# Performance work log

Measured on AMD Instinct MI355X. Metric: run time of the kernel, lower is better.

The kernel has to match this reference:

```python
import jax, jax.numpy as jnp
import numpy as np

N_NODES = 50000
N_EDGES = 800000
NODE_DIM = 64
EDGE_DIM = 32
OUT_FEATS = 64


def setup_inputs() -> dict:
    key = jax.random.key(0)
    k1, k2, k3, k4, k5, k6, k7 = jax.random.split(key, 7)
    node_features = jax.random.normal(k1, (N_NODES, NODE_DIM), dtype=jnp.float32)
    edge_features = jax.random.normal(k2, (N_EDGES, EDGE_DIM), dtype=jnp.float32)
    src = jax.random.randint(k3, (N_EDGES,), 0, N_NODES, dtype=jnp.int32)
    dst = jax.random.randint(k4, (N_EDGES,), 0, N_NODES, dtype=jnp.int32)
    in_dim = 2 * NODE_DIM + EDGE_DIM  # concat([e_ft, h_src, h_dst])
    w_group = jax.random.normal(k5, (in_dim,), dtype=jnp.float32) * 0.05
    w_srcattn = jax.random.normal(k6, (NODE_DIM + EDGE_DIM,), dtype=jnp.float32) * 0.05
    w_lin = jax.random.normal(k7, (in_dim, OUT_FEATS), dtype=jnp.float32) * 0.05
    return {"node_features": node_features, "edge_features": edge_features,
            "src": src, "dst": dst,
            "w_group": w_group, "w_srcattn": w_srcattn, "w_lin": w_lin}


def _segment_softmax(scores, seg, num_segments):
    # numerically-stable softmax of per-edge scalar scores within each segment
    m = jax.ops.segment_max(scores, seg, num_segments=num_segments)
    e = jnp.exp(scores - m[seg])
    s = jax.ops.segment_sum(e, seg, num_segments=num_segments)
    return e / s[seg]


def reference(node_features, edge_features, src, dst, w_group, w_srcattn, w_lin):
    h = node_features              # [N, node_dim]
    e_ft = edge_features           # [E, edge_dim]
    h_src = h[src]                 # [E, node_dim]
    h_dst = h[dst]                 # [E, node_dim]

    # --- group_apply_edges(group_by='src'): edge attention over out-edges of each src ---
    z2 = jnp.concatenate([e_ft, h_src, h_dst], axis=1)      # [E, edge_dim + 2*node_dim]
    a = z2 @ w_group                                        # [E]
    gamma = _segment_softmax(a, src, N_NODES)               # softmax over edges sharing src
    e_weighted = gamma[:, None] * e_ft                      # [E, edge_dim]

    # --- gnn_msg: msg = concat([h_src, e_weighted]) ---
    msg = jnp.concatenate([h_src, e_weighted], axis=1)      # [E, node_dim + edge_dim]

    # --- gnn_reduce: attention softmax over mailbox (edges sharing dst), weighted sum ---
    s = msg @ w_srcattn                                     # [E]
    alpha = _segment_softmax(s, dst, N_NODES)
    accum = jax.ops.segment_sum(alpha[:, None] * msg, dst, num_segments=N_NODES)  # [N, node_dim+edge_dim]

    # --- node_update: linear(concat([h, accum])) + relu ---
    h_cat = jnp.concatenate([h, accum], axis=1)             # [N, 2*node_dim + edge_dim]
    out = jax.nn.relu(h_cat @ w_lin)                        # [N, out_feats]
    return out
```

## Files before the change

kernel.cpp:

```cpp
#include <hip/hip_runtime.h>

#define NN 50000
#define NE 800000
#define NHB 3125
#define NTILES 3125

typedef __attribute__((ext_vector_type(8))) short bf16x8;
typedef __attribute__((ext_vector_type(4))) float f32x4;

static __device__ __forceinline__ short f2bf(float f) {
    unsigned int u = __float_as_uint(f);
    u += 0x7FFFu + ((u >> 16) & 1u);
    return (short)(u >> 16);
}

__global__ __launch_bounds__(256) void k_pre(
    const float* __restrict__ h, const int* __restrict__ dst,
    const float* __restrict__ wg, const float* __restrict__ wa,
    int* __restrict__ cnt, int* __restrict__ rank,
    float* __restrict__ p1, float* __restrict__ pd, float* __restrict__ dpf)
{
    int tid = threadIdx.x;
    if (blockIdx.x < NHB) {
        int e = blockIdx.x * 256 + tid;
        if (e < NE) rank[e] = atomicAdd(&cnt[dst[e]], 1);
        return;
    }
    __shared__ float4 ls[16], ld[16], lt[16];
    if (tid < 16)      ls[tid]      = ((const float4*)wg)[8 + tid];
    else if (tid < 32) ld[tid - 16] = ((const float4*)wg)[8 + tid];
    else if (tid < 48) lt[tid - 32] = ((const float4*)wa)[tid - 32];
    __syncthreads();
    int n = (blockIdx.x - NHB) * 16 + (tid >> 4);
    if (n >= NN) return;
    int l16 = tid & 15;
    float4 v = ((const float4*)(h + (size_t)n * 64))[l16];
    float4 w1 = ls[l16], w2 = ld[l16], w3 = lt[l16];
    float s1 = v.x*w1.x + v.y*w1.y + v.z*w1.z + v.w*w1.w;
    float s2 = v.x*w2.x + v.y*w2.y + v.z*w2.z + v.w*w2.w;
    float s3 = v.x*w3.x + v.y*w3.y + v.z*w3.z + v.w*w3.w;
    #pragma unroll
    for (int m = 8; m; m >>= 1) {
        s1 += __shfl_xor(s1, m);
        s2 += __shfl_xor(s2, m);
        s3 += __shfl_xor(s3, m);
    }
    if (l16 == 0) { p1[n] = s1; pd[n] = s2; dpf[2 * n + 1] = s3; }
}

__global__ __launch_bounds__(256) void k_assign(
    const int* __restrict__ cnt, int* __restrict__ off, int* __restrict__ gtotal)
{
    int n = blockIdx.x * 256 + threadIdx.x;
    int lane = threadIdx.x & 63;
    int c = (n < NN) ? cnt[n] : 0;
    int pre = c;
    #pragma unroll
    for (int d = 1; d < 64; d <<= 1) {
        int v = __shfl_up(pre, d);
        if (lane >= d) pre += v;
    }
    int base = 0;
    if (lane == 63) base = atomicAdd(gtotal, pre);
    base = __shfl(base, 63);
    if (n < NN) off[n] = base + pre - c;
}

__global__ __launch_bounds__(256) void k_edge(
    const float* __restrict__ ef, const int* __restrict__ src,
    const int* __restrict__ dst, const int* __restrict__ rank,
    const float* __restrict__ wg, const float* __restrict__ wa,
    const float* __restrict__ p1, const float* __restrict__ pd,
    float* __restrict__ dpf, const int* __restrict__ off,
    int4* __restrict__ recA)
{
    __shared__ float4 lwe[8], lae[8];
    int tid = threadIdx.x;
    if (tid < 8)       lwe[tid]     = ((const float4*)wg)[tid];
    else if (tid < 16) lae[tid - 8] = ((const float4*)wa)[tid - 8 + 16];
    __syncthreads();
    int e = blockIdx.x * 256 + tid;
    if (e >= NE) return;
    int s = src[e], d = dst[e], rk = rank[e];
    const float4* e4 = (const float4*)(ef + (size_t)e * 32);
    float a = 0.f, u = 0.f;
    #pragma unroll
    for (int q = 0; q < 8; ++q) {
        float4 v = e4[q], w = lwe[q], w2 = lae[q];
        a += v.x*w.x  + v.y*w.y  + v.z*w.z  + v.w*w.w;
        u += v.x*w2.x + v.y*w2.y + v.z*w2.z + v.w*w2.w;
    }
    a += p1[s] + pd[d];
    float eav = __expf(a);
    atomicAdd(&dpf[2 * s], eav);
    int pos = off[d] + rk;
    recA[pos] = make_int4(s, e, __float_as_int(eav), __float_as_int(u));
}

__global__ __launch_bounds__(256) void k_reduce(
    const float* __restrict__ h, const float* __restrict__ ef,
    const int* __restrict__ cnt, const int* __restrict__ off,
    const float2* __restrict__ dp, const int4* __restrict__ recA,
    float* __restrict__ accum)
{
    int n = blockIdx.x * 4 + (threadIdx.x >> 6);
    if (n >= NN) return;
    int lane = threadIdx.x & 63;
    bool up = lane >= 32;
    int l5 = lane & 31;
    int deg = cnt[n], base = off[n];
    float acch = 0.f, acce = 0.f, den = 0.f;
    int j = 0;
    for (; j + 4 <= deg; j += 4) {
        int4 r0 = recA[base+j+0], r1 = recA[base+j+1];
        int4 r2 = recA[base+j+2], r3 = recA[base+j+3];
        float2 d0 = dp[r0.x], d1 = dp[r1.x], d2 = dp[r2.x], d3 = dp[r3.x];
        float h0 = h[(size_t)r0.x*64+lane], h1 = h[(size_t)r1.x*64+lane];
        float h2 = h[(size_t)r2.x*64+lane], h3 = h[(size_t)r3.x*64+lane];
        int eA = up ? r1.y : r0.y, eB = up ? r3.y : r2.y;
        float efA = ef[(size_t)eA*32 + l5];
        float efB = ef[(size_t)eB*32 + l5];
        float g0 = __int_as_float(r0.z)/d0.x, g1 = __int_as_float(r1.z)/d1.x;
        float g2 = __int_as_float(r2.z)/d2.x, g3 = __int_as_float(r3.z)/d3.x;
        float s0 = __expf(d0.y + g0*__int_as_float(r0.w));
        float s1 = __expf(d1.y + g1*__int_as_float(r1.w));
        float s2 = __expf(d2.y + g2*__int_as_float(r2.w));
        float s3 = __expf(d3.y + g3*__int_as_float(r3.w));
        den  += s0 + s1 + s2 + s3;
        acch += s0*h0 + s1*h1 + s2*h2 + s3*h3;
        float wA = up ? s1*g1 : s0*g0;
        float wB = up ? s3*g3 : s2*g2;
        acce += wA*efA + wB*efB;
    }
    for (; j < deg; ++j) {
        int4 r = recA[base+j];
        float2 dt = dp[r.x];
        float g = __int_as_float(r.z)/dt.x;
        float s = __expf(dt.y + g*__int_as_float(r.w));
        den += s;
        acch += s * h[(size_t)r.x*64+lane];
        if (!up) acce += s * g * ef[(size_t)r.y*32 + l5];
    }
    acce += __shfl_xor(acce, 32);
    float inv = (deg > 0) ? 1.f/den : 0.f;
    accum[(size_t)n*96 + lane] = acch * inv;
    if (!up) accum[(size_t)n*96 + 64 + lane] = acce * inv;
}

__global__ __launch_bounds__(256) void k_node_update(
    const float* __restrict__ h, const float* __restrict__ accum,
    const float* __restrict__ wl_g, float* __restrict__ out)
{
    int lane = threadIdx.x & 63;
    int col  = lane & 15;
    int quad = lane >> 4;
    int wid  = blockIdx.x * 4 + (threadIdx.x >> 6);
    int nwaves = gridDim.x * 4;

    bf16x8 bfr[5][4];
    #pragma unroll
    for (int kc = 0; kc < 5; ++kc)
        #pragma unroll
        for (int nt = 0; nt < 4; ++nt) {
            #pragma unroll
            for (int j = 0; j < 8; ++j) {
                int k = kc * 32 + quad * 8 + j;
                bfr[kc][nt][j] = f2bf(wl_g[k * 64 + nt * 16 + col]);
            }
        }

    for (int tile = wid; tile < NTILES; tile += nwaves) {
        int n = tile * 16 + col;
        f32x4 acc[4];
        #pragma unroll
        for (int nt = 0; nt < 4; ++nt) acc[nt] = (f32x4){0.f, 0.f, 0.f, 0.f};

        #pragma unroll
        for (int kc = 0; kc < 5; ++kc) {
            int kbase = kc * 32 + quad * 8;
            const float* p = (kbase < 64)
                ? (h     + (size_t)n * 64 + kbase)
                : (accum + (size_t)n * 96 + (kbase - 64));
            float4 va = *(const float4*)p;
            float4 vb = *(const float4*)(p + 4);
            bf16x8 af;
            af[0] = f2bf(va.x); af[1] = f2bf(va.y);
            af[2] = f2bf(va.z); af[3] = f2bf(va.w);
            af[4] = f2bf(vb.x); af[5] = f2bf(vb.y);
            af[6] = f2bf(vb.z); af[7] = f2bf(vb.w);
            #pragma unroll
            for (int nt = 0; nt < 4; ++nt)
                acc[nt] = __builtin_amdgcn_mfma_f32_16x16x32_bf16(
                    af, bfr[kc][nt], acc[nt], 0, 0, 0);
        }

        #pragma unroll
        for (int nt = 0; nt < 4; ++nt) {
            #pragma unroll
            for (int r = 0; r < 4; ++r) {
                int node = tile * 16 + quad * 4 + r;
                out[(size_t)node * 64 + nt * 16 + col] = fmaxf(acc[nt][r], 0.f);
            }
        }
    }
}

extern "C" void kernel_launch(void* const* d_in, const int* in_sizes, int n_in,
                              void* d_out, int out_size, void* d_ws, size_t ws_size,
                              hipStream_t stream)
{
    const float* h   = (const float*)d_in[0];
    const float* ef  = (const float*)d_in[1];
    const int*   src = (const int*)d_in[2];
    const int*   dst = (const int*)d_in[3];
    const float* wg  = (const float*)d_in[4];
    const float* wa  = (const float*)d_in[5];
    const float* wl  = (const float*)d_in[6];
    float* out = (float*)d_out;

    float* ws = (float*)d_ws;
    float*  dpf    = ws;
    int*    cnt    = (int*)(ws + 2 * NN);
    int*    gtotal = (int*)(ws + 3 * NN);
    int*    off    = (int*)(ws + 3 * NN + 16);
    float*  p1     = ws + 4 * NN + 16;
    float*  pd     = ws + 5 * NN + 16;
    int4*   recA   = (int4*)(ws + 6 * NN + 16);
    int*    rank   = (int*)(ws + 6 * NN + 16 + 4 * NE);
    float*  accum  = ws + 6 * NN + 16 + 4 * NE;

    hipMemsetAsync(d_ws, 0, (size_t)(3 * NN + 16) * sizeof(float), stream);

    k_pre<<<2 * NHB, 256, 0, stream>>>(h, dst, wg, wa, cnt, rank, p1, pd, dpf);
    k_assign<<<(NN + 255) / 256, 256, 0, stream>>>(cnt, off, gtotal);
    k_edge<<<NHB, 256, 0, stream>>>(ef, src, dst, rank, wg, wa, p1, pd, dpf,
                                    off, recA);
    k_reduce<<<(NN + 3) / 4, 256, 0, stream>>>(h, ef, cnt, off, (const float2*)dpf,
                                               recA, accum);
    k_node_update<<<256, 256, 0, stream>>>(h, accum, wl, out);
}
```

Baseline: 336.6 us.

## Precompute per-edge softmax weights in a rewrite pass and move edge dots into pre-kernel

The edge-feature dot products (attention score part and srcattn part) move into the first kernel as a third block range, so they run alongside the degree histogram and are stored as a float2 per edge. A new k_rewrite pass runs once per record after the src-softmax denominators are complete. It computes gamma and exp(s) and stores exp(s) and exp(s)*gamma in recA. This removes the per-record dp gather, divide and exp from the reduce loop, where all 64 lanes of a wave repeated them. In exchange it adds an extra kernel launch, extra global traffic for the au buffer, and a full read-modify-write of recA. Bounds checks are also dropped because the sizes divide evenly.

Measured after the change: 346.2 us. 2.9% more time.

```diff
diff --git a/kernel.cpp b/kernel.cpp
--- a/kernel.cpp
+++ b/kernel.cpp
@@ -3,7 +3,6 @@
 #define NN 50000
 #define NE 800000
 #define NHB 3125
-#define NTILES 3125
 
 typedef __attribute__((ext_vector_type(8))) short bf16x8;
 typedef __attribute__((ext_vector_type(4))) float f32x4;
@@ -15,37 +14,55 @@
 }
 
 __global__ __launch_bounds__(256) void k_pre(
-    const float* __restrict__ h, const int* __restrict__ dst,
+    const float* __restrict__ h, const float* __restrict__ ef,
+    const int* __restrict__ dst,
     const float* __restrict__ wg, const float* __restrict__ wa,
     int* __restrict__ cnt, int* __restrict__ rank,
-    float* __restrict__ p1, float* __restrict__ pd, float* __restrict__ dpf)
+    float* __restrict__ p1, float* __restrict__ pd, float* __restrict__ dpf,
+    float2* __restrict__ au)
 {
     int tid = threadIdx.x;
     if (blockIdx.x < NHB) {
         int e = blockIdx.x * 256 + tid;
-        if (e < NE) rank[e] = atomicAdd(&cnt[dst[e]], 1);
+        rank[e] = atomicAdd(&cnt[dst[e]], 1);
         return;
     }
-    __shared__ float4 ls[16], ld[16], lt[16];
-    if (tid < 16)      ls[tid]      = ((const float4*)wg)[8 + tid];
-    else if (tid < 32) ld[tid - 16] = ((const float4*)wg)[8 + tid];
-    else if (tid < 48) lt[tid - 32] = ((const float4*)wa)[tid - 32];
+    if (blockIdx.x < 2 * NHB) {
+        __shared__ float4 ls[16], ld[16], lt[16];
+        if (tid < 16)      ls[tid]      = ((const float4*)wg)[8 + tid];
+        else if (tid < 32) ld[tid - 16] = ((const float4*)wg)[8 + tid];
+        else if (tid < 48) lt[tid - 32] = ((const float4*)wa)[tid - 32];
+        __syncthreads();
+        int n = (blockIdx.x - NHB) * 16 + (tid >> 4);
+        int l16 = tid & 15;
+        float4 v = ((const float4*)(h + (size_t)n * 64))[l16];
+        float4 w1 = ls[l16], w2 = ld[l16], w3 = lt[l16];
+        float s1 = v.x*w1.x + v.y*w1.y + v.z*w1.z + v.w*w1.w;
+        float s2 = v.x*w2.x + v.y*w2.y + v.z*w2.z + v.w*w2.w;
+        float s3 = v.x*w3.x + v.y*w3.y + v.z*w3.z + v.w*w3.w;
+        #pragma unroll
+        for (int m = 8; m; m >>= 1) {
+            s1 += __shfl_xor(s1, m);
+            s2 += __shfl_xor(s2, m);
+            s3 += __shfl_xor(s3, m);
+        }
+        if (l16 == 0) { p1[n] = s1; pd[n] = s2; dpf[2 * n + 1] = s3; }
+        return;
+    }
+    __shared__ float4 lwe[8], lae[8];
+    if (tid < 8)       lwe[tid]     = ((const float4*)wg)[tid];
+    else if (tid < 16) lae[tid - 8] = ((const float4*)wa)[tid - 8 + 16];
     __syncthreads();
-    int n = (blockIdx.x - NHB) * 16 + (tid >> 4);
-    if (n >= NN) return;
-    int l16 = tid & 15;
-    float4 v = ((const float4*)(h + (size_t)n * 64))[l16];
-    float4 w1 = ls[l16], w2 = ld[l16], w3 = lt[l16];
-    float s1 = v.x*w1.x + v.y*w1.y + v.z*w1.z + v.w*w1.w;
-    float s2 = v.x*w2.x + v.y*w2.y + v.z*w2.z + v.w*w2.w;
-    float s3 = v.x*w3.x + v.y*w3.y + v.z*w3.z + v.w*w3.w;
+    int e = (blockIdx.x - 2 * NHB) * 256 + tid;
+    const float4* e4 = (const float4*)(ef + (size_t)e * 32);
+    float a = 0.f, u = 0.f;
     #pragma unroll
-    for (int m = 8; m; m >>= 1) {
-        s1 += __shfl_xor(s1, m);
-        s2 += __shfl_xor(s2, m);
-        s3 += __shfl_xor(s3, m);
-    }
-    if (l16 == 0) { p1[n] = s1; pd[n] = s2; dpf[2 * n + 1] = s3; }
+    for (int q = 0; q < 8; ++q) {
+        float4 v = e4[q], w = lwe[q], w2 = lae[q];
+        a += v.x*w.x  + v.y*w.y  + v.z*w.z  + v.w*w.w;
+        u += v.x*w2.x + v.y*w2.y + v.z*w2.z + v.w*w2.w;
+    }
+    au[e] = make_float2(a, u);
 }
 
 __global__ __launch_bounds__(256) void k_assign(
@@ -67,44 +84,41 @@
 }
 
 __global__ __launch_bounds__(256) void k_edge(
-    const float* __restrict__ ef, const int* __restrict__ src,
+    const float2* __restrict__ au, const int* __restrict__ src,
     const int* __restrict__ dst, const int* __restrict__ rank,
-    const float* __restrict__ wg, const float* __restrict__ wa,
     const float* __restrict__ p1, const float* __restrict__ pd,
     float* __restrict__ dpf, const int* __restrict__ off,
     int4* __restrict__ recA)
 {
-    __shared__ float4 lwe[8], lae[8];
-    int tid = threadIdx.x;
-    if (tid < 8)       lwe[tid]     = ((const float4*)wg)[tid];
-    else if (tid < 16) lae[tid - 8] = ((const float4*)wa)[tid - 8 + 16];
-    __syncthreads();
-    int e = blockIdx.x * 256 + tid;
-    if (e >= NE) return;
+    int e = blockIdx.x * 256 + threadIdx.x;
     int s = src[e], d = dst[e], rk = rank[e];
-    const float4* e4 = (const float4*)(ef + (size_t)e * 32);
-    float a = 0.f, u = 0.f;
-    #pragma unroll
-    for (int q = 0; q < 8; ++q) {
-        float4 v = e4[q], w = lwe[q], w2 = lae[q];
-        a += v.x*w.x  + v.y*w.y  + v.z*w.z  + v.w*w.w;
-        u += v.x*w2.x + v.y*w2.y + v.z*w2.z + v.w*w2.w;
-    }
-    a += p1[s] + pd[d];
+    float2 ad = au[e];
+    float a = ad.x + p1[s] + pd[d];
     float eav = __expf(a);
     atomicAdd(&dpf[2 * s], eav);
     int pos = off[d] + rk;
-    recA[pos] = make_int4(s, e, __float_as_int(eav), __float_as_int(u));
+    recA[pos] = make_int4(s, e, __float_as_int(eav), __float_as_int(ad.y));
+}
+
+__global__ __launch_bounds__(256) void k_rewrite(
+    const float2* __restrict__ dp, int4* __restrict__ recA)
+{
+    int pos = blockIdx.x * 256 + threadIdx.x;
+    int4 r = recA[pos];
+    float2 dt = dp[r.x];
+    float g = __int_as_float(r.z) / dt.x;
+    float es = __expf(dt.y + g * __int_as_float(r.w));
+    r.z = __float_as_int(es);
+    r.w = __float_as_int(es * g);
+    recA[pos] = r;
 }
 
 __global__ __launch_bounds__(256) void k_reduce(
     const float* __restrict__ h, const float* __restrict__ ef,
     const int* __restrict__ cnt, const int* __restrict__ off,
-    const float2* __restrict__ dp, const int4* __restrict__ recA,
-    float* __restrict__ accum)
+    const int4* __restrict__ recA, float* __restrict__ accum)
 {
     int n = blockIdx.x * 4 + (threadIdx.x >> 6);
-    if (n >= NN) return;
     int lane = threadIdx.x & 63;
     bool up = lane >= 32;
     int l5 = lane & 31;
@@ -114,32 +128,25 @@
     for (; j + 4 <= deg; j += 4) {
         int4 r0 = recA[base+j+0], r1 = recA[base+j+1];
         int4 r2 = recA[base+j+2], r3 = recA[base+j+3];
-        float2 d0 = dp[r0.x], d1 = dp[r1.x], d2 = dp[r2.x], d3 = dp[r3.x];
         float h0 = h[(size_t)r0.x*64+lane], h1 = h[(size_t)r1.x*64+lane];
         float h2 = h[(size_t)r2.x*64+lane], h3 = h[(size_t)r3.x*64+lane];
         int eA = up ? r1.y : r0.y, eB = up ? r3.y : r2.y;
         float efA = ef[(size_t)eA*32 + l5];
         float efB = ef[(size_t)eB*32 + l5];
-        float g0 = __int_as_float(r0.z)/d0.x, g1 = __int_as_float(r1.z)/d1.x;
-        float g2 = __int_as_float(r2.z)/d2.x, g3 = __int_as_float(r3.z)/d3.x;
-        float s0 = __expf(d0.y + g0*__int_as_float(r0.w));
-        float s1 = __expf(d1.y + g1*__int_as_float(r1.w));
-        float s2 = __expf(d2.y + g2*__int_as_float(r2.w));
-        float s3 = __expf(d3.y + g3*__int_as_float(r3.w));
+        float s0 = __int_as_float(r0.z), s1 = __int_as_float(r1.z);
+        float s2 = __int_as_float(r2.z), s3 = __int_as_float(r3.z);
         den  += s0 + s1 + s2 + s3;
         acch += s0*h0 + s1*h1 + s2*h2 + s3*h3;
-        float wA = up ? s1*g1 : s0*g0;
-        float wB = up ? s3*g3 : s2*g2;
+        float wA = up ? __int_as_float(r1.w) : __int_as_float(r0.w);
+        float wB = up ? __int_as_float(r3.w) : __int_as_float(r2.w);
         acce += wA*efA + wB*efB;
     }
     for (; j < deg; ++j) {
         int4 r = recA[base+j];
-        float2 dt = dp[r.x];
-        float g = __int_as_float(r.z)/dt.x;
-        float s = __expf(dt.y + g*__int_as_float(r.w));
+        float s = __int_as_float(r.z);
         den += s;
         acch += s * h[(size_t)r.x*64+lane];
-        if (!up) acce += s * g * ef[(size_t)r.y*32 + l5];
+        if (!up) acce += __int_as_float(r.w) * ef[(size_t)r.y*32 + l5];
     }
     acce += __shfl_xor(acce, 32);
     float inv = (deg > 0) ? 1.f/den : 0.f;
@@ -169,7 +176,7 @@
             }
         }
 
-    for (int tile = wid; tile < NTILES; tile += nwaves) {
+    for (int tile = wid; tile < NHB; tile += nwaves) {
         int n = tile * 16 + col;
         f32x4 acc[4];
         #pragma unroll
@@ -226,16 +233,17 @@
     float*  p1     = ws + 4 * NN + 16;
     float*  pd     = ws + 5 * NN + 16;
     int4*   recA   = (int4*)(ws + 6 * NN + 16);
-    int*    rank   = (int*)(ws + 6 * NN + 16 + 4 * NE);
+    float2* au     = (float2*)(ws + 6 * NN + 16 + 4 * NE);
+    int*    rank   = (int*)(ws + 6 * NN + 16 + 4 * NE + 2 * NE);
     float*  accum  = ws + 6 * NN + 16 + 4 * NE;
 
     hipMemsetAsync(d_ws, 0, (size_t)(3 * NN + 16) * sizeof(float), stream);
 
-    k_pre<<<2 * NHB, 256, 0, stream>>>(h, dst, wg, wa, cnt, rank, p1, pd, dpf);
+    k_pre<<<3 * NHB, 256, 0, stream>>>(h, ef, dst, wg, wa, cnt, rank, p1, pd,
+                                       dpf, au);
     k_assign<<<(NN + 255) / 256, 256, 0, stream>>>(cnt, off, gtotal);
-    k_edge<<<NHB, 256, 0, stream>>>(ef, src, dst, rank, wg, wa, p1, pd, dpf,
-                                    off, recA);
-    k_reduce<<<(NN + 3) / 4, 256, 0, stream>>>(h, ef, cnt, off, (const float2*)dpf,
-                                               recA, accum);
+    k_edge<<<NHB, 256, 0, stream>>>(au, src, dst, rank, p1, pd, dpf, off, recA);
+    k_rewrite<<<NHB, 256, 0, stream>>>((const float2*)dpf, recA);
+    k_reduce<<<NN / 4, 256, 0, stream>>>(h, ef, cnt, off, recA, accum);
     k_node_update<<<256, 256, 0, stream>>>(h, accum, wl, out);
 }
```
